# Optimization experiments

Hardware: AMD Instinct MI355X
Metric: run time of the kernel (lower is better)

## Reference

```python
import jax, jax.numpy as jnp
import numpy as np

REG_COEF = 25.0  # reg_coef from __init__


def _chamfer_bidir_sum(x, y):
    # x: [B,N,3], y: [B,M,3] -> scalar: sum over batch/points of bidirectional
    # nearest-neighbor squared distances (point_reduction='sum', batch_reduction='sum')
    d = jnp.sum((x[:, :, None, :] - y[:, None, :, :]) ** 2, axis=-1)  # [B,N,M]
    return jnp.sum(jnp.min(d, axis=2)) + jnp.sum(jnp.min(d, axis=1))


def _reflect(points, planes):
    # points: [B,N,3], planes: [B,4] -> reflected points [B,N,3]
    n = planes[:, :3] / jnp.linalg.norm(planes[:, :3], axis=1, keepdims=True)  # [B,3]
    off = planes[:, 3]
    dist = jnp.einsum('bd,bnd->bn', n, points) + off[:, None]  # signed distance [B,N]
    return points - 2.0 * dist[:, :, None] * n[:, None, :]


def setup_inputs() -> dict:
    key = jax.random.key(0)
    k1, k2 = jax.random.split(key)
    sample_points = jax.random.normal(k1, (8, 4096, 3), dtype=jnp.float32)
    y_pred = jax.random.normal(k2, (8, 3, 4), dtype=jnp.float32)
    return {"sample_points": sample_points, "y_pred": y_pred}


def reference(sample_points, y_pred):
    B, H, _ = y_pred.shape
    # regularization: Frobenius norm of (N N^T - I) per batch, summed
    normals = y_pred[:, :, :3]
    normals = normals / jnp.linalg.norm(normals, axis=2, keepdims=True)  # [B,H,3]
    gram = jnp.einsum('bcd,bed->bce', normals, normals) - jnp.eye(H, dtype=normals.dtype)
    reg = jnp.sum(jnp.sqrt(jnp.sum(gram ** 2, axis=(1, 2))))
    # reflection (symmetry-distance) loss, looped over the small fixed head count
    refl = jnp.zeros((), dtype=sample_points.dtype)
    for h in range(H):
        reflected = _reflect(sample_points, y_pred[:, h, :])
        refl = refl + _chamfer_bidir_sum(sample_points, reflected)
    return refl + REG_COEF * reg
```

## Files before the change

### kernel.cpp

```cpp
#include <hip/hip_runtime.h>
#include <math.h>

#define REG_COEF 25.0f
#define B 8
#define H 3
#define N 4096

typedef _Float16 f16x8 __attribute__((ext_vector_type(8)));
typedef float f32x16 __attribute__((ext_vector_type(16)));

static constexpr int NX = B * N;
static constexpr int NY = B * H * N;
static constexpr int NM = 2 * B * H * N;


__global__ void prep_kernel(const float* __restrict__ pts, const float* __restrict__ ypred,
                            char* __restrict__ ApkX, char* __restrict__ BpkX,
                            char* __restrict__ ApkY, char* __restrict__ BpkY,
                            float* __restrict__ mins, float* __restrict__ out)
{
    int idx = blockIdx.x * blockDim.x + threadIdx.x;
    if (idx == 0) {
        float reg = 0.f;
        for (int b = 0; b < B; ++b) {
            float n[H][3];
            #pragma unroll
            for (int h = 0; h < H; ++h) {
                float a0 = ypred[b * 12 + h * 4 + 0];
                float a1 = ypred[b * 12 + h * 4 + 1];
                float a2 = ypred[b * 12 + h * 4 + 2];
                float inv = rsqrtf(a0 * a0 + a1 * a1 + a2 * a2);
                n[h][0] = a0 * inv; n[h][1] = a1 * inv; n[h][2] = a2 * inv;
            }
            float s = 0.f;
            #pragma unroll
            for (int c = 0; c < H; ++c)
                #pragma unroll
                for (int e = 0; e < H; ++e) {
                    float g = n[c][0] * n[e][0] + n[c][1] * n[e][1] + n[c][2] * n[e][2];
                    if (c == e) g -= 1.f;
                    s += g * g;
                }
            reg += sqrtf(s);
        }
        out[0] = REG_COEF * reg;
    }

    union { _Float16 h[16]; uint4 u[2]; } pa, pb;

    if (idx < NX) {
        const float* p = pts + (size_t)idx * 3;
        float x = p[0], y = p[1], z = p[2];
        float w = x * x + y * y + z * z;
        float ax = -2.f * x, ay = -2.f * y, az = -2.f * z;
        _Float16 ahx = (_Float16)ax, ahy = (_Float16)ay, ahz = (_Float16)az;
        _Float16 wh = (_Float16)w;
        pa.h[0] = ahx; pa.h[1] = ahy; pa.h[2] = ahz;
        pa.h[3] = (_Float16)(ax - (float)ahx);
        pa.h[4] = (_Float16)(ay - (float)ahy);
        pa.h[5] = (_Float16)(az - (float)ahz);
        pa.h[6] = ahx; pa.h[7] = ahy; pa.h[8] = ahz;
        pa.h[9] = wh; pa.h[10] = (_Float16)(w - (float)wh);
        pa.h[11] = (_Float16)1.f; pa.h[12] = (_Float16)1.f;
        pa.h[13] = (_Float16)0.f; pa.h[14] = (_Float16)0.f; pa.h[15] = (_Float16)0.f;
        ((uint4*)(ApkX + (size_t)idx * 32))[0] = pa.u[0];
        ((uint4*)(ApkX + (size_t)idx * 32))[1] = pa.u[1];
        _Float16 thx = (_Float16)x, thy = (_Float16)y, thz = (_Float16)z;
        pb.h[0] = thx; pb.h[1] = thy; pb.h[2] = thz;
        pb.h[3] = thx; pb.h[4] = thy; pb.h[5] = thz;
        pb.h[6] = (_Float16)(x - (float)thx);
        pb.h[7] = (_Float16)(y - (float)thy);
        pb.h[8] = (_Float16)(z - (float)thz);
        pb.h[9] = (_Float16)1.f; pb.h[10] = (_Float16)1.f;
        pb.h[11] = wh; pb.h[12] = (_Float16)(w - (float)wh);
        pb.h[13] = (_Float16)0.f; pb.h[14] = (_Float16)0.f; pb.h[15] = (_Float16)0.f;
        ((uint4*)(BpkX + (size_t)idx * 32))[0] = pb.u[0];
        ((uint4*)(BpkX + (size_t)idx * 32))[1] = pb.u[1];
    } else if (idx < NX + NY) {
        int t = idx - NX;
        int nn = t & (N - 1);
        int bh = t >> 12;
        int b = bh / H, h = bh - b * H;
        float a0 = ypred[b * 12 + h * 4 + 0];
        float a1 = ypred[b * 12 + h * 4 + 1];
        float a2 = ypred[b * 12 + h * 4 + 2];
        float off = ypred[b * 12 + h * 4 + 3];
        float inv = rsqrtf(a0 * a0 + a1 * a1 + a2 * a2);
        a0 *= inv; a1 *= inv; a2 *= inv;
        const float* p = pts + ((size_t)b * N + nn) * 3;
        float x0 = p[0], x1 = p[1], x2 = p[2];
        float dist = a0 * x0 + a1 * x1 + a2 * x2 + off;
        float x = fmaf(-2.f * dist, a0, x0);
        float y = fmaf(-2.f * dist, a1, x1);
        float z = fmaf(-2.f * dist, a2, x2);
        float w = x * x + y * y + z * z;
        _Float16 thx = (_Float16)x, thy = (_Float16)y, thz = (_Float16)z;
        _Float16 wh = (_Float16)w;
        pb.h[0] = thx; pb.h[1] = thy; pb.h[2] = thz;
        pb.h[3] = thx; pb.h[4] = thy; pb.h[5] = thz;
        pb.h[6] = (_Float16)(x - (float)thx);
        pb.h[7] = (_Float16)(y - (float)thy);
        pb.h[8] = (_Float16)(z - (float)thz);
        pb.h[9] = (_Float16)1.f; pb.h[10] = (_Float16)1.f;
        pb.h[11] = wh; pb.h[12] = (_Float16)(w - (float)wh);
        pb.h[13] = (_Float16)0.f; pb.h[14] = (_Float16)0.f; pb.h[15] = (_Float16)0.f;
        ((uint4*)(BpkY + (size_t)t * 32))[0] = pb.u[0];
        ((uint4*)(BpkY + (size_t)t * 32))[1] = pb.u[1];
        float ax = -2.f * x, ay = -2.f * y, az = -2.f * z;
        _Float16 ahx = (_Float16)ax, ahy = (_Float16)ay, ahz = (_Float16)az;
        pa.h[0] = ahx; pa.h[1] = ahy; pa.h[2] = ahz;
        pa.h[3] = (_Float16)(ax - (float)ahx);
        pa.h[4] = (_Float16)(ay - (float)ahy);
        pa.h[5] = (_Float16)(az - (float)ahz);
        pa.h[6] = ahx; pa.h[7] = ahy; pa.h[8] = ahz;
        pa.h[9] = wh; pa.h[10] = (_Float16)(w - (float)wh);
        pa.h[11] = (_Float16)1.f; pa.h[12] = (_Float16)1.f;
        pa.h[13] = (_Float16)0.f; pa.h[14] = (_Float16)0.f; pa.h[15] = (_Float16)0.f;
        ((uint4*)(ApkY + (size_t)t * 32))[0] = pa.u[0];
        ((uint4*)(ApkY + (size_t)t * 32))[1] = pa.u[1];
    } else if (idx < NX + NY + NM) {
        mins[idx - NX - NY] = __uint_as_float(0x7F800000u);
    }
}

__global__ __launch_bounds__(256, 4) void chamfer_kernel(const char* __restrict__ ApkX,
                                                         const char* __restrict__ BpkX,
                                                         const char* __restrict__ ApkY,
                                                         const char* __restrict__ BpkY,
                                                         float* __restrict__ mins)
{
    int bid = blockIdx.x;
    int ts = bid & 1;
    int qs = (bid >> 1) & 15;
    int rest = bid >> 5;
    int hh = rest % 3;
    int tmp = rest / 3;
    int b = tmp & 7;
    int dir = tmp >> 3;

    int tid = threadIdx.x;
    int w = tid >> 6;
    int lane = tid & 63;
    int l31 = lane & 31, kb = lane >> 5;

    const char* Aq;
    const char* Bt;
    float* mq_base;
    if (dir == 0) {
        Aq = ApkX + (size_t)b * N * 32;
        Bt = BpkY + (size_t)(b * H + hh) * N * 32;
        mq_base = mins + (size_t)(b * H + hh) * N;
    } else {
        Aq = ApkY + (size_t)(b * H + hh) * N * 32;
        Bt = BpkX + (size_t)b * N * 32;
        mq_base = mins + (size_t)B * H * N + (size_t)(b * H + hh) * N;
    }
    int qbase = qs * 256 + w * 64;
    Aq += (size_t)qbase * 32;
    Bt += (size_t)ts * 2048 * 32;

    f16x8 A0 = *(const f16x8*)(Aq + ((size_t)(l31)) * 32 + kb * 16);
    f16x8 A1 = *(const f16x8*)(Aq + ((size_t)(32 + l31)) * 32 + kb * 16);

    f32x16 mq0, mq1;
    #pragma unroll
    for (int r = 0; r < 16; ++r) { mq0[r] = INFINITY; mq1[r] = INFINITY; }

    const char* Bp = Bt + (size_t)l31 * 32 + kb * 16;
    f16x8 B0 = *(const f16x8*)(Bp);
    f16x8 B1 = *(const f16x8*)(Bp + 1024);
    f32x16 zero = {};

    for (int bt = 0; bt < 64; bt += 2) {
        f16x8 Bn0 = *(const f16x8*)(Bp + (size_t)(bt + 2) * 1024);
        f16x8 Bn1 = *(const f16x8*)(Bp + (size_t)(bt + 3) * 1024);
        f32x16 D0 = __builtin_amdgcn_mfma_f32_32x32x16_f16(A0, B0, zero, 0, 0, 0);
        f32x16 D1 = __builtin_amdgcn_mfma_f32_32x32x16_f16(A0, B1, zero, 0, 0, 0);
        #pragma unroll
        for (int r = 0; r < 16; ++r)
            mq0[r] = fminf(mq0[r], fminf(D0[r], D1[r]));
        f32x16 D2 = __builtin_amdgcn_mfma_f32_32x32x16_f16(A1, B0, zero, 0, 0, 0);
        f32x16 D3 = __builtin_amdgcn_mfma_f32_32x32x16_f16(A1, B1, zero, 0, 0, 0);
        #pragma unroll
        for (int r = 0; r < 16; ++r)
            mq1[r] = fminf(mq1[r], fminf(D2[r], D3[r]));
        B0 = Bn0; B1 = Bn1;
    }

    #pragma unroll
    for (int a = 0; a < 2; ++a) {
        #pragma unroll
        for (int r = 0; r < 16; ++r) {
            float v = (a == 0) ? mq0[r] : mq1[r];
            v = fminf(v, __shfl_xor(v, 1, 64));
            v = fminf(v, __shfl_xor(v, 2, 64));
            v = fminf(v, __shfl_xor(v, 4, 64));
            v = fminf(v, __shfl_xor(v, 8, 64));
            v = fminf(v, __shfl_xor(v, 16, 64));
            if (l31 == 0) {
                int row = (r & 3) + 8 * (r >> 2) + 4 * kb;
                atomicMin((unsigned*)&mq_base[qbase + a * 32 + row],
                          __float_as_uint(fmaxf(v, 0.f)));
            }
        }
    }
}

__global__ void reduce_kernel(const float* __restrict__ mins, float* __restrict__ out)
{
    int tid = blockIdx.x * blockDim.x + threadIdx.x;
    float s = 0.f;
    #pragma unroll
    for (int k = 0; k < 4; ++k) s += mins[tid + k * 49152];
    #pragma unroll
    for (int off = 32; off > 0; off >>= 1) s += __shfl_down(s, off);
    if ((threadIdx.x & 63) == 0) atomicAdd(out, s);
}

extern "C" void kernel_launch(void* const* d_in, const int* in_sizes, int n_in,
                              void* d_out, int out_size, void* d_ws, size_t ws_size,
                              hipStream_t stream)
{
    const float* pts = (const float*)d_in[0];
    const float* yp  = (const float*)d_in[1];
    float* out = (float*)d_out;
    float* ws  = (float*)d_ws;

    char* ApkX = (char*)ws;
    char* BpkX = (char*)(ws + 262144);
    char* ApkY = (char*)(ws + 524288);
    char* BpkY = (char*)(ws + 1310720);
    float* mins = ws + 2097152;

    prep_kernel<<<1280, 256, 0, stream>>>(pts, yp, ApkX, BpkX, ApkY, BpkY, mins, out);
    chamfer_kernel<<<1536, 256, 0, stream>>>(ApkX, BpkX, ApkY, BpkY, mins);
    reduce_kernel<<<192, 256, 0, stream>>>(mins, out);
}
```

Before: 65.09 us.

## Switch chamfer MFMA from 32x32x16 to 16x16x32 tiles with 64-byte packing

Repacks the point operands to 32 halves (64 bytes) per point and rewrites the chamfer inner loop to use 16x16x32 f16 MFMA. Each wave now keeps four 16-row A fragments and walks twice as many 16-column B tiles. The end-of-loop reduction becomes a four-step shuffle with more atomics per row. The aim is a smaller accumulator footprint and a cheaper final reduction. In exchange, the padded K dimension doubles the MFMA work and the packed-buffer memory traffic, since only 13 of the 32 halves carry data.

```diff
diff --git a/kernel.cpp b/kernel.cpp
--- a/kernel.cpp
+++ b/kernel.cpp
@@ -7,7 +7,7 @@
 #define N 4096
 
 typedef _Float16 f16x8 __attribute__((ext_vector_type(8)));
-typedef float f32x16 __attribute__((ext_vector_type(16)));
+typedef float f32x4 __attribute__((ext_vector_type(4)));
 
 static constexpr int NX = B * N;
 static constexpr int NY = B * H * N;
@@ -46,12 +46,14 @@
         out[0] = REG_COEF * reg;
     }
 
-    union { _Float16 h[16]; uint4 u[2]; } pa, pb;
+    union { _Float16 h[32]; uint4 u[4]; } pa, pb;
 
     if (idx < NX) {
         const float* p = pts + (size_t)idx * 3;
         float x = p[0], y = p[1], z = p[2];
         float w = x * x + y * y + z * z;
+        #pragma unroll
+        for (int i = 0; i < 32; ++i) { pa.h[i] = (_Float16)0.f; pb.h[i] = (_Float16)0.f; }
         float ax = -2.f * x, ay = -2.f * y, az = -2.f * z;
         _Float16 ahx = (_Float16)ax, ahy = (_Float16)ay, ahz = (_Float16)az;
         _Float16 wh = (_Float16)w;
@@ -62,9 +64,8 @@
         pa.h[6] = ahx; pa.h[7] = ahy; pa.h[8] = ahz;
         pa.h[9] = wh; pa.h[10] = (_Float16)(w - (float)wh);
         pa.h[11] = (_Float16)1.f; pa.h[12] = (_Float16)1.f;
-        pa.h[13] = (_Float16)0.f; pa.h[14] = (_Float16)0.f; pa.h[15] = (_Float16)0.f;
-        ((uint4*)(ApkX + (size_t)idx * 32))[0] = pa.u[0];
-        ((uint4*)(ApkX + (size_t)idx * 32))[1] = pa.u[1];
+        uint4* da = (uint4*)(ApkX + (size_t)idx * 64);
+        da[0] = pa.u[0]; da[1] = pa.u[1]; da[2] = pa.u[2]; da[3] = pa.u[3];
         _Float16 thx = (_Float16)x, thy = (_Float16)y, thz = (_Float16)z;
         pb.h[0] = thx; pb.h[1] = thy; pb.h[2] = thz;
         pb.h[3] = thx; pb.h[4] = thy; pb.h[5] = thz;
@@ -73,9 +74,8 @@
         pb.h[8] = (_Float16)(z - (float)thz);
         pb.h[9] = (_Float16)1.f; pb.h[10] = (_Float16)1.f;
         pb.h[11] = wh; pb.h[12] = (_Float16)(w - (float)wh);
-        pb.h[13] = (_Float16)0.f; pb.h[14] = (_Float16)0.f; pb.h[15] = (_Float16)0.f;
-        ((uint4*)(BpkX + (size_t)idx * 32))[0] = pb.u[0];
-        ((uint4*)(BpkX + (size_t)idx * 32))[1] = pb.u[1];
+        uint4* db = (uint4*)(BpkX + (size_t)idx * 64);
+        db[0] = pb.u[0]; db[1] = pb.u[1]; db[2] = pb.u[2]; db[3] = pb.u[3];
     } else if (idx < NX + NY) {
         int t = idx - NX;
         int nn = t & (N - 1);
@@ -94,6 +94,8 @@
         float y = fmaf(-2.f * dist, a1, x1);
         float z = fmaf(-2.f * dist, a2, x2);
         float w = x * x + y * y + z * z;
+        #pragma unroll
+        for (int i = 0; i < 32; ++i) { pa.h[i] = (_Float16)0.f; pb.h[i] = (_Float16)0.f; }
         _Float16 thx = (_Float16)x, thy = (_Float16)y, thz = (_Float16)z;
         _Float16 wh = (_Float16)w;
         pb.h[0] = thx; pb.h[1] = thy; pb.h[2] = thz;
@@ -103,9 +105,8 @@
         pb.h[8] = (_Float16)(z - (float)thz);
         pb.h[9] = (_Float16)1.f; pb.h[10] = (_Float16)1.f;
         pb.h[11] = wh; pb.h[12] = (_Float16)(w - (float)wh);
-        pb.h[13] = (_Float16)0.f; pb.h[14] = (_Float16)0.f; pb.h[15] = (_Float16)0.f;
-        ((uint4*)(BpkY + (size_t)t * 32))[0] = pb.u[0];
-        ((uint4*)(BpkY + (size_t)t * 32))[1] = pb.u[1];
+        uint4* db = (uint4*)(BpkY + (size_t)t * 64);
+        db[0] = pb.u[0]; db[1] = pb.u[1]; db[2] = pb.u[2]; db[3] = pb.u[3];
         float ax = -2.f * x, ay = -2.f * y, az = -2.f * z;
         _Float16 ahx = (_Float16)ax, ahy = (_Float16)ay, ahz = (_Float16)az;
         pa.h[0] = ahx; pa.h[1] = ahy; pa.h[2] = ahz;
@@ -115,9 +116,8 @@
         pa.h[6] = ahx; pa.h[7] = ahy; pa.h[8] = ahz;
         pa.h[9] = wh; pa.h[10] = (_Float16)(w - (float)wh);
         pa.h[11] = (_Float16)1.f; pa.h[12] = (_Float16)1.f;
-        pa.h[13] = (_Float16)0.f; pa.h[14] = (_Float16)0.f; pa.h[15] = (_Float16)0.f;
-        ((uint4*)(ApkY + (size_t)t * 32))[0] = pa.u[0];
-        ((uint4*)(ApkY + (size_t)t * 32))[1] = pa.u[1];
+        uint4* da = (uint4*)(ApkY + (size_t)t * 64);
+        da[0] = pa.u[0]; da[1] = pa.u[1]; da[2] = pa.u[2]; da[3] = pa.u[3];
     } else if (idx < NX + NY + NM) {
         mins[idx - NX - NY] = __uint_as_float(0x7F800000u);
     }
@@ -141,65 +141,66 @@
     int tid = threadIdx.x;
     int w = tid >> 6;
     int lane = tid & 63;
-    int l31 = lane & 31, kb = lane >> 5;
+    int c16 = lane & 15, g4 = lane >> 4;
 
     const char* Aq;
     const char* Bt;
     float* mq_base;
     if (dir == 0) {
-        Aq = ApkX + (size_t)b * N * 32;
-        Bt = BpkY + (size_t)(b * H + hh) * N * 32;
+        Aq = ApkX + (size_t)b * N * 64;
+        Bt = BpkY + (size_t)(b * H + hh) * N * 64;
         mq_base = mins + (size_t)(b * H + hh) * N;
     } else {
-        Aq = ApkY + (size_t)(b * H + hh) * N * 32;
-        Bt = BpkX + (size_t)b * N * 32;
+        Aq = ApkY + (size_t)(b * H + hh) * N * 64;
+        Bt = BpkX + (size_t)b * N * 64;
         mq_base = mins + (size_t)B * H * N + (size_t)(b * H + hh) * N;
     }
     int qbase = qs * 256 + w * 64;
-    Aq += (size_t)qbase * 32;
-    Bt += (size_t)ts * 2048 * 32;
-
-    f16x8 A0 = *(const f16x8*)(Aq + ((size_t)(l31)) * 32 + kb * 16);
-    f16x8 A1 = *(const f16x8*)(Aq + ((size_t)(32 + l31)) * 32 + kb * 16);
-
-    f32x16 mq0, mq1;
-    #pragma unroll
-    for (int r = 0; r < 16; ++r) { mq0[r] = INFINITY; mq1[r] = INFINITY; }
-
-    const char* Bp = Bt + (size_t)l31 * 32 + kb * 16;
+    Aq += (size_t)qbase * 64;
+    Bt += (size_t)ts * 2048 * 64;
+
+    f16x8 A[4];
+    #pragma unroll
+    for (int af = 0; af < 4; ++af)
+        A[af] = *(const f16x8*)(Aq + (size_t)(af * 16 + c16) * 64 + g4 * 16);
+
+    f32x4 mq[4];
+    #pragma unroll
+    for (int af = 0; af < 4; ++af)
+        #pragma unroll
+        for (int r = 0; r < 4; ++r) mq[af][r] = INFINITY;
+
+    const char* Bp = Bt + (size_t)c16 * 64 + g4 * 16;
     f16x8 B0 = *(const f16x8*)(Bp);
     f16x8 B1 = *(const f16x8*)(Bp + 1024);
-    f32x16 zero = {};
-
-    for (int bt = 0; bt < 64; bt += 2) {
+    f32x4 zero = {};
+
+    for (int bt = 0; bt < 128; bt += 2) {
         f16x8 Bn0 = *(const f16x8*)(Bp + (size_t)(bt + 2) * 1024);
         f16x8 Bn1 = *(const f16x8*)(Bp + (size_t)(bt + 3) * 1024);
-        f32x16 D0 = __builtin_amdgcn_mfma_f32_32x32x16_f16(A0, B0, zero, 0, 0, 0);
-        f32x16 D1 = __builtin_amdgcn_mfma_f32_32x32x16_f16(A0, B1, zero, 0, 0, 0);
-        #pragma unroll
-        for (int r = 0; r < 16; ++r)
-            mq0[r] = fminf(mq0[r], fminf(D0[r], D1[r]));
-        f32x16 D2 = __builtin_amdgcn_mfma_f32_32x32x16_f16(A1, B0, zero, 0, 0, 0);
-        f32x16 D3 = __builtin_amdgcn_mfma_f32_32x32x16_f16(A1, B1, zero, 0, 0, 0);
-        #pragma unroll
-        for (int r = 0; r < 16; ++r)
-            mq1[r] = fminf(mq1[r], fminf(D2[r], D3[r]));
+        #pragma unroll
+        for (int af = 0; af < 4; ++af) {
+            f32x4 D0 = __builtin_amdgcn_mfma_f32_16x16x32_f16(A[af], B0, zero, 0, 0, 0);
+            f32x4 D1 = __builtin_amdgcn_mfma_f32_16x16x32_f16(A[af], B1, zero, 0, 0, 0);
+            #pragma unroll
+            for (int r = 0; r < 4; ++r)
+                mq[af][r] = fminf(mq[af][r], fminf(D0[r], D1[r]));
+        }
         B0 = Bn0; B1 = Bn1;
     }
 
     #pragma unroll
-    for (int a = 0; a < 2; ++a) {
-        #pragma unroll
-        for (int r = 0; r < 16; ++r) {
-            float v = (a == 0) ? mq0[r] : mq1[r];
+    for (int af = 0; af < 4; ++af) {
+        #pragma unroll
+        for (int r = 0; r < 4; ++r) {
+            float v = mq[af][r];
             v = fminf(v, __shfl_xor(v, 1, 64));
             v = fminf(v, __shfl_xor(v, 2, 64));
             v = fminf(v, __shfl_xor(v, 4, 64));
             v = fminf(v, __shfl_xor(v, 8, 64));
-            v = fminf(v, __shfl_xor(v, 16, 64));
-            if (l31 == 0) {
-                int row = (r & 3) + 8 * (r >> 2) + 4 * kb;
-                atomicMin((unsigned*)&mq_base[qbase + a * 32 + row],
+            if (c16 == 0) {
+                int row = g4 * 4 + r;
+                atomicMin((unsigned*)&mq_base[qbase + af * 16 + row],
                           __float_as_uint(fmaxf(v, 0.f)));
             }
         }
@@ -224,13 +225,13 @@
     const float* pts = (const float*)d_in[0];
     const float* yp  = (const float*)d_in[1];
     float* out = (float*)d_out;
-    float* ws  = (float*)d_ws;
-
-    char* ApkX = (char*)ws;
-    char* BpkX = (char*)(ws + 262144);
-    char* ApkY = (char*)(ws + 524288);
-    char* BpkY = (char*)(ws + 1310720);
-    float* mins = ws + 2097152;
+    char* ws   = (char*)d_ws;
+
+    char* ApkX = ws;
+    char* BpkX = ws + (2u << 20);
+    char* ApkY = ws + (4u << 20);
+    char* BpkY = ws + (10u << 20);
+    float* mins = (float*)(ws + (16u << 20));
 
     prep_kernel<<<1280, 256, 0, stream>>>(pts, yp, ApkX, BpkX, ApkY, BpkY, mins, out);
     chamfer_kernel<<<1536, 256, 0, stream>>>(ApkX, BpkX, ApkY, BpkY, mins);
```

After: 82.51 us. 26.8% more time.
